# Performance work log

Measured on AMD Instinct MI355X. Metric: run time of the kernel, lower is better.

## Reference

```python
import jax, jax.numpy as jnp
import numpy as np

NP, NA, H, K, TAU = 4096, 2048, 128, 5, 1.0
NODE_N = {'paper': NP, 'author': NA}
RELS = [('pp', 'paper', 'paper'), ('aa', 'author', 'author'),
        ('pa', 'paper', 'author'), ('ap', 'author', 'paper')]


def setup_inputs():
    key = jax.random.key(0)
    ks = jax.random.split(key, 32)
    f32 = jnp.float32
    def nrm(k, shape, scale=1.0):
        return jax.random.normal(k, shape, f32) * scale
    Epp, Eaa, Epa, Eap = 131072, 65536, 131072, 131072
    inp = {
        'x_paper': nrm(ks[0], (NP, H)),
        'x_author': nrm(ks[1], (NA, H)),
        'ei_pp': jax.random.randint(ks[2], (2, Epp), 0, NP, dtype=jnp.int32),
        'ei_aa': jax.random.randint(ks[3], (2, Eaa), 0, NA, dtype=jnp.int32),
        'ei_pa': jnp.stack([jax.random.randint(ks[4], (Epa,), 0, NP, dtype=jnp.int32),
                            jax.random.randint(ks[5], (Epa,), 0, NA, dtype=jnp.int32)]),
        'ei_ap': jnp.stack([jax.random.randint(ks[6], (Eap,), 0, NA, dtype=jnp.int32),
                            jax.random.randint(ks[7], (Eap,), 0, NP, dtype=jnp.int32)]),
        'batch_paper': jnp.zeros((NP,), jnp.int32),
        'batch_author': jnp.zeros((NA,), jnp.int32),
        'index': 7,
    }
    s = H ** -0.5
    i = 8
    for t in ('paper', 'author'):
        for l in (0, 1):
            inp['Wself_%s%d' % (t, l)] = nrm(ks[i], (H, H), s); i += 1
    for r, _, _ in RELS:
        for l in (0, 1):
            inp['W%s%d' % (r, l)] = nrm(ks[i], (H, H), s); i += 1
    for r in ('pp', 'aa'):
        inp['Wep1_%s' % r] = nrm(ks[i], (2 * H, 256), (2 * H) ** -0.5); i += 1
        inp['bep1_%s' % r] = jnp.zeros((256,), f32)
        inp['Wep2_%s' % r] = nrm(ks[i], (256, 2), 256 ** -0.5); i += 1
        inp['bep2_%s' % r] = jnp.zeros((2,), f32)
    inp['Wc'] = nrm(ks[i], (H, 5), s)
    inp['bc'] = jnp.zeros((5,), f32)
    return inp


def _mean_agg(msg, dst, n):
    s = jax.ops.segment_sum(msg, dst, num_segments=n)
    c = jax.ops.segment_sum(jnp.ones((msg.shape[0], 1), msg.dtype), dst, num_segments=n)
    return s / jnp.maximum(c, 1.0)


def _gnn(x, ei, p, single, edge_attn=None):
    # 2-layer relation-typed mean-aggregation hetero GNN.
    h = dict(x)
    for l in (0, 1):
        nh = {}
        for t in ('paper', 'author'):
            agg = h[t] @ p['Wself_%s%d' % (t, l)]
            for r, s_t, d_t in RELS:
                if d_t != t or (single and s_t != d_t):
                    continue
                src, dst = ei[r][0], ei[r][1]
                msg = h[s_t][src] @ p['W%s%d' % (r, l)]  # [E, H]
                if edge_attn is not None and r in edge_attn:
                    msg = msg * edge_attn[r][:, None]
                agg = agg + _mean_agg(msg, dst, NODE_N[t])
            nh[t] = jax.nn.relu(agg)
        h = nh
    return h


def _edge_pred(h, ei, p, r, t):
    src, dst = ei[r][0], ei[r][1]
    e = jnp.concatenate([h[t][src], h[t][dst]], axis=-1)  # [E, 2H]
    e = jax.nn.relu(e @ p['Wep1_%s' % r] + p['bep1_%s' % r])
    return e @ p['Wep2_%s' % r] + p['bep2_%s' % r]  # [E, 2]


def _gumbel_topk(logits, mask, k, tau, key):
    # Masked straight-through top-k gumbel-softmax (row-wise, hard=True).
    u = jax.random.uniform(key, logits.shape, logits.dtype, 1e-10, 1.0)
    g = -jnp.log(-jnp.log(u))
    y = jnp.where(mask, (logits + g) / tau, -1e9)
    soft = jax.nn.softmax(y, axis=-1)
    _, idx = jax.lax.top_k(soft, k)  # [N, k]
    rows = jnp.arange(logits.shape[0])[:, None]
    hard = jnp.zeros_like(soft).at[rows, idx].set(1.0)
    return hard - jax.lax.stop_gradient(soft) + soft


def _prune(h, ei, p, r, t, n, key):
    pred = _edge_pred(h, ei, p, r, t)[:, 0]
    src, dst = ei[r][0], ei[r][1]
    # sparse_coo_tensor(...).to_dense(): duplicates coalesce by sum
    A = jnp.zeros((n, n), pred.dtype).at[src, dst].add(pred)
    S = _gumbel_topk(A, A > 0, K, TAU, key)
    return S[src, dst]


def _forward(p, ints):
    x = {'paper': p['x_paper'], 'author': p['x_author']}
    ei = {'pp': ints['ei_pp'], 'aa': ints['ei_aa'], 'pa': ints['ei_pa'], 'ap': ints['ei_ap']}
    h1 = _gnn(x, ei, p, single=True)
    kpp, kaa = jax.random.split(jax.random.key(42))
    w_pp = _prune(h1, ei, p, 'pp', 'paper', NP, kpp)
    w_aa = _prune(h1, ei, p, 'aa', 'author', NA, kaa)
    h2 = _gnn(x, ei, p, single=False, edge_attn={'pp': w_pp, 'aa': w_aa})
    pool = h2['paper'][ints['index']].reshape(1, -1)
    y_hat = pool @ p['Wc'] + p['bc']
    return y_hat, w_pp, w_aa


def reference(x_paper, x_author, ei_pp, ei_aa, ei_pa, ei_ap, batch_paper, batch_author, index,
              Wself_paper0, Wself_paper1, Wself_author0, Wself_author1,
              Wpp0, Wpp1, Waa0, Waa1, Wpa0, Wpa1, Wap0, Wap1,
              Wep1_pp, bep1_pp, Wep2_pp, bep2_pp, Wep1_aa, bep1_aa, Wep2_aa, bep2_aa,
              Wc, bc):
    p = dict(x_paper=x_paper, x_author=x_author,
             Wself_paper0=Wself_paper0, Wself_paper1=Wself_paper1,
             Wself_author0=Wself_author0, Wself_author1=Wself_author1,
             Wpp0=Wpp0, Wpp1=Wpp1, Waa0=Waa0, Waa1=Waa1,
             Wpa0=Wpa0, Wpa1=Wpa1, Wap0=Wap0, Wap1=Wap1,
             Wep1_pp=Wep1_pp, bep1_pp=bep1_pp, Wep2_pp=Wep2_pp, bep2_pp=bep2_pp,
             Wep1_aa=Wep1_aa, bep1_aa=bep1_aa, Wep2_aa=Wep2_aa, bep2_aa=bep2_aa,
             Wc=Wc, bc=bc)
    ints = dict(ei_pp=ei_pp, ei_aa=ei_aa, ei_pa=ei_pa, ei_ap=ei_ap, index=index)
    return _forward(p, ints)
```

## Files before the change

kernel.cpp:

```cpp
#include <hip/hip_runtime.h>
#include <stdint.h>


namespace {

constexpr int NPn = 4096;
constexpr int NAn = 2048;
constexpr int Hh  = 128;
constexpr int EPPc = 131072;
constexpr int EAAc = 65536;
constexpr int KSEL = 5;
constexpr int BSLOT = 128;


__host__ __device__ static inline void tf2x32(uint32_t k0, uint32_t k1,
                                              uint32_t& x0, uint32_t& x1) {
  uint32_t ks2 = k0 ^ k1 ^ 0x1BD11BDAu;
  x0 += k0; x1 += k1;
#define TF_R(r) { x0 += x1; x1 = (x1 << (r)) | (x1 >> (32 - (r))); x1 ^= x0; }
  TF_R(13) TF_R(15) TF_R(26) TF_R(6)
  x0 += k1;  x1 += ks2 + 1u;
  TF_R(17) TF_R(29) TF_R(16) TF_R(24)
  x0 += ks2; x1 += k0 + 2u;
  TF_R(13) TF_R(15) TF_R(26) TF_R(6)
  x0 += k0;  x1 += k1 + 3u;
  TF_R(17) TF_R(29) TF_R(16) TF_R(24)
  x0 += k1;  x1 += ks2 + 4u;
  TF_R(13) TF_R(15) TF_R(26) TF_R(6)
  x0 += ks2; x1 += k0 + 5u;
#undef TF_R
}

__global__ __launch_bounds__(256) void scatter_kernel(
    const int* src_pp, const int* dst_pp, const int* src_aa, const int* dst_aa,
    const int* src_pa, const int* dst_pa, const int* src_ap, const int* dst_ap,
    int* cnt, int* entries)
{
  int i = blockIdx.x * 256 + threadIdx.x;
  int key, pl;
  if (i < 131072) {
    int e = i;
    key = 0 + dst_pp[e]; pl = (src_pp[e] << 18) | e;
  } else if (i < 196608) {
    int e = i - 131072;
    key = 4096 + dst_aa[e]; pl = (src_aa[e] << 16) | e;
  } else if (i < 327680) {
    int e = i - 196608;
    key = 6144 + dst_pa[e]; pl = src_pa[e];
  } else if (i < 458752) {
    int e = i - 327680;
    key = 8192 + dst_ap[e]; pl = src_ap[e];
  } else if (i < 589824) {
    int e = i - 458752;
    key = 12288 + src_pp[e]; pl = (dst_pp[e] << 18) | e;
  } else if (i < 655360) {
    int e = i - 589824;
    key = 16384 + src_aa[e]; pl = (dst_aa[e] << 16) | e;
  } else return;
  int pos = atomicAdd(&cnt[key], 1);
  if (pos < BSLOT) entries[key * BSLOT + pos] = pl;
}

struct AggSeg { const float* h; const float* w; float* M; int cntOff; int shift; };
struct AggArgs { AggSeg s[4]; int start[5]; int nseg; };

__global__ __launch_bounds__(256) void multi_agg(AggArgs a, const int* __restrict__ cnt,
                                                 const int* __restrict__ entries)
{
  int g = blockIdx.x * 8 + (threadIdx.x >> 5);
  int fl = (threadIdx.x & 31) << 2;
  if (g >= a.start[a.nseg]) return;
  int si = 0;
  while (si < a.nseg - 1 && g >= a.start[si + 1]) ++si;
  AggSeg sg = a.s[si];
  int node = g - a.start[si];
  int deg = cnt[sg.cntOff + node];
  const int* ent = entries + (size_t)(sg.cntOff + node) * BSLOT;
  int b = 0, e = deg;
  const float* h = sg.h;
  int sh = sg.shift;
  float ax = 0.f, ay = 0.f, az = 0.f, aw = 0.f;
  if (sg.w) {
    unsigned mask = (1u << sh) - 1u;
    int k = b;
    for (; k + 3 < e; k += 4) {
      unsigned p0 = (unsigned)ent[k], p1 = (unsigned)ent[k + 1];
      unsigned p2 = (unsigned)ent[k + 2], p3 = (unsigned)ent[k + 3];
      float w0 = sg.w[p0 & mask], w1 = sg.w[p1 & mask];
      float w2v = sg.w[p2 & mask], w3 = sg.w[p3 & mask];
      float4 v0, v1, v2, v3;
      if (w0 != 0.f) v0 = *(const float4*)&h[(size_t)(p0 >> sh) * Hh + fl];
      if (w1 != 0.f) v1 = *(const float4*)&h[(size_t)(p1 >> sh) * Hh + fl];
      if (w2v != 0.f) v2 = *(const float4*)&h[(size_t)(p2 >> sh) * Hh + fl];
      if (w3 != 0.f) v3 = *(const float4*)&h[(size_t)(p3 >> sh) * Hh + fl];
      if (w0 != 0.f) { ax += v0.x; ay += v0.y; az += v0.z; aw += v0.w; }
      if (w1 != 0.f) { ax += v1.x; ay += v1.y; az += v1.z; aw += v1.w; }
      if (w2v != 0.f) { ax += v2.x; ay += v2.y; az += v2.z; aw += v2.w; }
      if (w3 != 0.f) { ax += v3.x; ay += v3.y; az += v3.z; aw += v3.w; }
    }
    for (; k < e; ++k) {
      unsigned pl = (unsigned)ent[k];
      float wt = sg.w[pl & mask];
      if (wt != 0.f) {
        float4 v = *(const float4*)&h[(size_t)(pl >> sh) * Hh + fl];
        ax += v.x; ay += v.y; az += v.z; aw += v.w;
      }
    }
  } else {
    int k = b;
    for (; k + 7 < e; k += 8) {
      unsigned p0 = (unsigned)ent[k],     p1 = (unsigned)ent[k + 1];
      unsigned p2 = (unsigned)ent[k + 2], p3 = (unsigned)ent[k + 3];
      unsigned p4 = (unsigned)ent[k + 4], p5 = (unsigned)ent[k + 5];
      unsigned p6 = (unsigned)ent[k + 6], p7 = (unsigned)ent[k + 7];
      float4 v0 = *(const float4*)&h[(size_t)(p0 >> sh) * Hh + fl];
      float4 v1 = *(const float4*)&h[(size_t)(p1 >> sh) * Hh + fl];
      float4 v2 = *(const float4*)&h[(size_t)(p2 >> sh) * Hh + fl];
      float4 v3 = *(const float4*)&h[(size_t)(p3 >> sh) * Hh + fl];
      float4 v4 = *(const float4*)&h[(size_t)(p4 >> sh) * Hh + fl];
      float4 v5 = *(const float4*)&h[(size_t)(p5 >> sh) * Hh + fl];
      float4 v6 = *(const float4*)&h[(size_t)(p6 >> sh) * Hh + fl];
      float4 v7 = *(const float4*)&h[(size_t)(p7 >> sh) * Hh + fl];
      ax += v0.x; ay += v0.y; az += v0.z; aw += v0.w;
      ax += v1.x; ay += v1.y; az += v1.z; aw += v1.w;
      ax += v2.x; ay += v2.y; az += v2.z; aw += v2.w;
      ax += v3.x; ay += v3.y; az += v3.z; aw += v3.w;
      ax += v4.x; ay += v4.y; az += v4.z; aw += v4.w;
      ax += v5.x; ay += v5.y; az += v5.z; aw += v5.w;
      ax += v6.x; ay += v6.y; az += v6.z; aw += v6.w;
      ax += v7.x; ay += v7.y; az += v7.z; aw += v7.w;
    }
    for (; k < e; ++k) {
      unsigned pl = (unsigned)ent[k];
      float4 v = *(const float4*)&h[(size_t)(pl >> sh) * Hh + fl];
      ax += v.x; ay += v.y; az += v.z; aw += v.w;
    }
  }
  float cd = fmaxf((float)deg, 1.0f);
  float4 o; o.x = ax / cd; o.y = ay / cd; o.z = az / cd; o.w = aw / cd;
  *(float4*)&sg.M[(size_t)node * Hh + fl] = o;
}

struct GDesc {
  const float* A0; const float* W0; const float* A1; const float* W1;
  const float* A2; const float* W2; float* C; int M; int N; int parts; int relu;
};
struct GArgs { GDesc d[4]; int bstart[5]; int nd; };

__global__ __launch_bounds__(256) void gemm_b(GArgs g)
{
  __shared__ __align__(16) float As[2][32][68];
  __shared__ __align__(16) float Ws[2][32][68];
  int blk = blockIdx.x;
  int di = 0;
  while (di < g.nd - 1 && blk >= g.bstart[di + 1]) ++di;
  GDesc D = g.d[di];
  int local = blk - g.bstart[di];
  int nTiles = D.N >> 6;
  int bx = local % nTiles;
  int by = local / nTiles;
  int m0 = by << 6, n0 = bx << 6;
  int N = D.N;
  int tid = threadIdx.x;
  int tr = tid >> 4, tc = tid & 15;
  int r = tid >> 3, f = tid & 7;
  float acc[4][4] = {{0.f}};
  const float* Ap[3] = {D.A0, D.A1, D.A2};
  const float* Wp[3] = {D.W0, D.W1, D.W2};
  int T = D.parts << 2;

  float4 va0, va1, vw0, vw1;
  auto ldchunk = [&](int t) {
    const float* A = Ap[t >> 2]; const float* W = Wp[t >> 2];
    int k0 = (t & 3) << 5;
    va0 = *(const float4*)&A[(size_t)(m0 + r) * 128 + k0 + f * 4];
    va1 = *(const float4*)&A[(size_t)(m0 + r + 32) * 128 + k0 + f * 4];
    vw0 = *(const float4*)&W[(size_t)(k0 + r) * N + n0 + f * 4];
    vw1 = *(const float4*)&W[(size_t)(k0 + r) * N + n0 + f * 4 + 32];
  };
  auto stchunk = [&](int buf) {
    As[buf][f * 4 + 0][r] = va0.x; As[buf][f * 4 + 1][r] = va0.y;
    As[buf][f * 4 + 2][r] = va0.z; As[buf][f * 4 + 3][r] = va0.w;
    As[buf][f * 4 + 0][r + 32] = va1.x; As[buf][f * 4 + 1][r + 32] = va1.y;
    As[buf][f * 4 + 2][r + 32] = va1.z; As[buf][f * 4 + 3][r + 32] = va1.w;
    *(float4*)&Ws[buf][r][f * 4] = vw0;
    *(float4*)&Ws[buf][r][f * 4 + 32] = vw1;
  };

  ldchunk(0);
  stchunk(0);
  __syncthreads();
  for (int t = 0; t < T; ++t) {
    int cur = t & 1;
    bool more = (t + 1 < T);
    if (more) ldchunk(t + 1);
#pragma unroll
    for (int k = 0; k < 32; ++k) {
      float4 a = *(const float4*)&As[cur][k][tr * 4];
      float4 b = *(const float4*)&Ws[cur][k][tc * 4];
      acc[0][0] += a.x * b.x; acc[0][1] += a.x * b.y; acc[0][2] += a.x * b.z; acc[0][3] += a.x * b.w;
      acc[1][0] += a.y * b.x; acc[1][1] += a.y * b.y; acc[1][2] += a.y * b.z; acc[1][3] += a.y * b.w;
      acc[2][0] += a.z * b.x; acc[2][1] += a.z * b.y; acc[2][2] += a.z * b.z; acc[2][3] += a.z * b.w;
      acc[3][0] += a.w * b.x; acc[3][1] += a.w * b.y; acc[3][2] += a.w * b.z; acc[3][3] += a.w * b.w;
    }
    if (more) stchunk(cur ^ 1);
    __syncthreads();
  }
#pragma unroll
  for (int i = 0; i < 4; ++i) {
    float4 v;
    v.x = acc[i][0]; v.y = acc[i][1]; v.z = acc[i][2]; v.w = acc[i][3];
    if (D.relu) {
      v.x = fmaxf(v.x, 0.f); v.y = fmaxf(v.y, 0.f);
      v.z = fmaxf(v.z, 0.f); v.w = fmaxf(v.w, 0.f);
    }
    *(float4*)&D.C[(size_t)(m0 + tr * 4 + i) * N + n0 + tc * 4] = v;
  }
}

__global__ __launch_bounds__(256) void row_topk(
    const float* __restrict__ P1pp, const float* __restrict__ P2pp,
    const float* __restrict__ b1pp, const float* __restrict__ W2pp,
    const float* __restrict__ b2pp,
    const float* __restrict__ P1aa, const float* __restrict__ P2aa,
    const float* __restrict__ b1aa, const float* __restrict__ W2aa,
    const float* __restrict__ b2aa,
    const int* __restrict__ cnt, const int* __restrict__ entries,
    float* __restrict__ w_pp, float* __restrict__ w_aa,
    uint32_t kpp0, uint32_t kpp1, uint32_t kaa0, uint32_t kaa1)
{
  __shared__ float P1s[256], b1s[256], w2s[256];
  __shared__ int   dS[128];
  __shared__ float pS[128];
  __shared__ int   sel5[KSEL];
  int blk = blockIdx.x, tid = threadIdx.x;
  int lane = tid & 63, wv = tid >> 6;
  int row, Ncols, shift, co; unsigned mask;
  const float* P1; const float* P2; const float* b1; const float* W2; const float* b2;
  float* wout; uint32_t k0, k1;
  if (blk < NPn) {
    row = blk; Ncols = NPn; shift = 18; mask = 0x3FFFFu; co = 12288;
    P1 = P1pp; P2 = P2pp; b1 = b1pp; W2 = W2pp; b2 = b2pp;
    wout = w_pp; k0 = kpp0; k1 = kpp1;
  } else {
    row = blk - NPn; Ncols = NAn; shift = 16; mask = 0xFFFFu; co = 16384;
    P1 = P1aa; P2 = P2aa; b1 = b1aa; W2 = W2aa; b2 = b2aa;
    wout = w_aa; k0 = kaa0; k1 = kaa1;
  }
  const int* ent = entries + (size_t)(co + row) * BSLOT;
  int deg = cnt[co + row];
  P1s[tid] = P1[(size_t)row * 256 + tid];
  b1s[tid] = b1[tid];
  w2s[tid] = W2[tid * 2];
  __syncthreads();
  float bias2 = b2[0];
  int j = lane << 2;
  for (int k = wv * 4; k < deg; k += 16) {
    int n = deg - k; if (n > 4) n = 4;
    unsigned pl0 = (unsigned)ent[k];
    unsigned pl1 = (n > 1) ? (unsigned)ent[k + 1] : pl0;
    unsigned pl2 = (n > 2) ? (unsigned)ent[k + 2] : pl0;
    unsigned pl3 = (n > 3) ? (unsigned)ent[k + 3] : pl0;
    int d0 = (int)(pl0 >> shift), d1 = (int)(pl1 >> shift);
    int d2 = (int)(pl2 >> shift), d3 = (int)(pl3 >> shift);
    float4 q0 = *(const float4*)&P2[(size_t)d0 * 256 + j];
    float4 q1 = *(const float4*)&P2[(size_t)d1 * 256 + j];
    float4 q2 = *(const float4*)&P2[(size_t)d2 * 256 + j];
    float4 q3 = *(const float4*)&P2[(size_t)d3 * 256 + j];
    float pa = P1s[j + 0], pb = P1s[j + 1], pc = P1s[j + 2], pd = P1s[j + 3];
    float ba = b1s[j + 0], bb = b1s[j + 1], bc_ = b1s[j + 2], bd = b1s[j + 3];
    float wa = w2s[j + 0], wb = w2s[j + 1], wc = w2s[j + 2], wd = w2s[j + 3];
    float s0 = fmaxf(pa + q0.x + ba, 0.f) * wa + fmaxf(pb + q0.y + bb, 0.f) * wb +
               fmaxf(pc + q0.z + bc_, 0.f) * wc + fmaxf(pd + q0.w + bd, 0.f) * wd;
    float s1 = fmaxf(pa + q1.x + ba, 0.f) * wa + fmaxf(pb + q1.y + bb, 0.f) * wb +
               fmaxf(pc + q1.z + bc_, 0.f) * wc + fmaxf(pd + q1.w + bd, 0.f) * wd;
    float s2 = fmaxf(pa + q2.x + ba, 0.f) * wa + fmaxf(pb + q2.y + bb, 0.f) * wb +
               fmaxf(pc + q2.z + bc_, 0.f) * wc + fmaxf(pd + q2.w + bd, 0.f) * wd;
    float s3 = fmaxf(pa + q3.x + ba, 0.f) * wa + fmaxf(pb + q3.y + bb, 0.f) * wb +
               fmaxf(pc + q3.z + bc_, 0.f) * wc + fmaxf(pd + q3.w + bd, 0.f) * wd;
    for (int off = 32; off; off >>= 1) {
      s0 += __shfl_down(s0, off);
      s1 += __shfl_down(s1, off);
      s2 += __shfl_down(s2, off);
      s3 += __shfl_down(s3, off);
    }
    if (lane == 0) {
      dS[k] = d0; pS[k] = s0 + bias2;
      if (n > 1) { dS[k + 1] = d1; pS[k + 1] = s1 + bias2; }
      if (n > 2) { dS[k + 2] = d2; pS[k + 2] = s2 + bias2; }
      if (n > 3) { dS[k + 3] = d3; pS[k + 3] = s3 + bias2; }
    }
  }
  __syncthreads();
  if (deg > 0 && wv == 0) {
    int   e0 = (lane < deg) ? dS[lane] : -1;
    float q0v = (lane < deg) ? pS[lane] : 0.f;
    bool  two = (deg > 64);
    int   e1 = -1; float q1v = 0.f;
    if (two && 64 + lane < deg) { e1 = dS[64 + lane]; q1v = pS[64 + lane]; }
    float a0 = 0.f, a1 = 0.f;
    bool lead0 = (e0 >= 0), lead1 = (e1 >= 0);
    for (int j2 = 0; j2 < deg; ++j2) {
      int bj; float bp;
      if (j2 < 64) { bj = __shfl(e0, j2); bp = __shfl(q0v, j2); }
      else         { bj = __shfl(e1, j2 - 64); bp = __shfl(q1v, j2 - 64); }
      if (e0 >= 0 && bj == e0) { a0 += bp; if (j2 < lane) lead0 = false; }
      if (e1 >= 0 && bj == e1) { a1 += bp; if (j2 < 64 + lane) lead1 = false; }
    }
    uint32_t rowbase = (uint32_t)row * (uint32_t)Ncols;
    float y0 = -1e9f, y1 = -1e9f;
    bool c0 = lead0 && (a0 > 0.f);
    if (c0) {
      uint32_t x0 = 0u, x1 = rowbase + (uint32_t)e0;
      tf2x32(k0, k1, x0, x1);
      uint32_t bits = x0 ^ x1;
      float fv = __uint_as_float((bits >> 9) | 0x3f800000u) - 1.0f;
      float u = fmaxf(1e-10f, fv + 1e-10f);
      y0 = a0 + (-logf(-logf(u)));
    }
    bool c1 = lead1 && (a1 > 0.f);
    if (c1) {
      uint32_t x0 = 0u, x1 = rowbase + (uint32_t)e1;
      tf2x32(k0, k1, x0, x1);
      uint32_t bits = x0 ^ x1;
      float fv = __uint_as_float((bits >> 9) | 0x3f800000u) - 1.0f;
      float u = fmaxf(1e-10f, fv + 1e-10f);
      y1 = a1 + (-logf(-logf(u)));
    }
    int cnt2 = __popcll(__ballot(c0)) + __popcll(__ballot(c1));
    int nsel = cnt2 < KSEL ? cnt2 : KSEL;
    for (int it = 0; it < nsel; ++it) {
      float best; int bc;
      if (y1 > y0 || (y1 == y0 && (unsigned)e1 < (unsigned)e0)) { best = y1; bc = e1; }
      else { best = y0; bc = e0; }
      for (int m = 32; m; m >>= 1) {
        float ov = __shfl_xor(best, m); int oc = __shfl_xor(bc, m);
        if (ov > best || (ov == best && (unsigned)oc < (unsigned)bc)) { best = ov; bc = oc; }
      }
      if (lane == 0) sel5[it] = bc;
      if (e0 == bc) y0 = -3.0e38f;
      if (e1 == bc) y1 = -3.0e38f;
    }
    if (nsel < KSEL && lane == 0) {
      int c = 0;
      for (int it = nsel; it < KSEL; ++it) {
        for (;;) {
          bool used = false;
          for (int q = 0; q < it; ++q) used |= (sel5[q] == c);
          if (!used) break;
          ++c;
        }
        sel5[it] = c++;
      }
    }
  }
  __syncthreads();
  for (int k = tid; k < deg; k += 256) {
    unsigned pl = (unsigned)ent[k];
    int d = (int)(pl >> shift);
    int e = (int)(pl & mask);
    float v = 0.f;
#pragma unroll
    for (int q = 0; q < KSEL; ++q) v = (sel5[q] == d) ? 1.f : v;
    wout[e] = v;
  }
}

__global__ __launch_bounds__(128) void final_kernel(
    const float* __restrict__ hp, const float* __restrict__ ha,
    const int* __restrict__ idxPtr, const float* __restrict__ wpp,
    const int* __restrict__ cnt, const int* __restrict__ entries,
    const float* __restrict__ Wself, const float* __restrict__ Wpp,
    const float* __restrict__ Wap,
    const float* __restrict__ Wc, const float* __restrict__ bc,
    float* __restrict__ out)
{
  __shared__ float selfr[128], mpp[128], mapr[128], t[128];
  int tid = threadIdx.x;
  int idx = idxPtr[0];
  selfr[tid] = hp[(size_t)idx * 128 + tid];
  {
    int deg = cnt[idx];
    const int* ent = entries + (size_t)idx * BSLOT;
    float acc = 0.f;
    for (int k = 0; k < deg; ++k) {
      unsigned pl = (unsigned)ent[k];
      int s = (int)(pl >> 18);
      int e = (int)(pl & 0x3FFFFu);
      acc += wpp[e] * hp[(size_t)s * 128 + tid];
    }
    mpp[tid] = acc / fmaxf((float)deg, 1.0f);
  }
  {
    int deg = cnt[8192 + idx];
    const int* ent = entries + (size_t)(8192 + idx) * BSLOT;
    float acc = 0.f;
    for (int k = 0; k < deg; ++k) {
      int s = ent[k];
      acc += ha[(size_t)s * 128 + tid];
    }
    mapr[tid] = acc / fmaxf((float)deg, 1.0f);
  }
  __syncthreads();
  float s = 0.f;
  for (int m = 0; m < 128; ++m) {
    s += selfr[m] * Wself[m * 128 + tid] + mpp[m] * Wpp[m * 128 + tid] +
         mapr[m] * Wap[m * 128 + tid];
  }
  t[tid] = fmaxf(s, 0.f);
  __syncthreads();
  if (tid < 5) {
    float y = bc[tid];
    for (int k = 0; k < 128; ++k) y += t[k] * Wc[k * 5 + tid];
    out[tid] = y;
  }
}

}

extern "C" void kernel_launch(void* const* d_in, const int* in_sizes, int n_in,
                              void* d_out, int out_size, void* d_ws, size_t ws_size,
                              hipStream_t stream)
{
  (void)in_sizes; (void)n_in; (void)out_size; (void)ws_size;
  const float* x_p = (const float*)d_in[0];
  const float* x_a = (const float*)d_in[1];
  const int* ei_pp = (const int*)d_in[2];
  const int* ei_aa = (const int*)d_in[3];
  const int* ei_pa = (const int*)d_in[4];
  const int* ei_ap = (const int*)d_in[5];
  const int* idxPtr = (const int*)d_in[8];
  const float* Wself_p0 = (const float*)d_in[9];
  const float* Wself_p1 = (const float*)d_in[10];
  const float* Wself_a0 = (const float*)d_in[11];
  const float* Wself_a1 = (const float*)d_in[12];
  const float* Wpp0 = (const float*)d_in[13]; const float* Wpp1 = (const float*)d_in[14];
  const float* Waa0 = (const float*)d_in[15]; const float* Waa1 = (const float*)d_in[16];
  const float* Wpa0 = (const float*)d_in[17];
  const float* Wap0 = (const float*)d_in[19]; const float* Wap1 = (const float*)d_in[20];
  const float* Wep1_pp = (const float*)d_in[21]; const float* bep1_pp = (const float*)d_in[22];
  const float* Wep2_pp = (const float*)d_in[23]; const float* bep2_pp = (const float*)d_in[24];
  const float* Wep1_aa = (const float*)d_in[25]; const float* bep1_aa = (const float*)d_in[26];
  const float* Wep2_aa = (const float*)d_in[27]; const float* bep2_aa = (const float*)d_in[28];
  const float* Wc = (const float*)d_in[29]; const float* bc = (const float*)d_in[30];

  float* out = (float*)d_out;
  float* w_pp_out = out + 5;
  float* w_aa_out = out + 5 + EPPc;

  const int* src_pp = ei_pp;  const int* dst_pp = ei_pp + EPPc;
  const int* src_aa = ei_aa;  const int* dst_aa = ei_aa + EAAc;
  const int* src_pa = ei_pa;  const int* dst_pa = ei_pa + 131072;
  const int* src_ap = ei_ap;  const int* dst_ap = ei_ap + 131072;

  char* p = (char*)d_ws;
  auto alloc = [&](size_t bytes) -> void* {
    void* r = (void*)p;
    p += (bytes + 255) & ~(size_t)255;
    return r;
  };
  int* cnt     = (int*)alloc(18432 * sizeof(int));
  int* entries = (int*)alloc((size_t)18432 * BSLOT * sizeof(int));
  float* Mpp  = (float*)alloc((size_t)NPn * Hh * sizeof(float));
  float* Maa  = (float*)alloc((size_t)NAn * Hh * sizeof(float));
  float* Mpa  = (float*)alloc((size_t)NAn * Hh * sizeof(float));
  float* Map  = (float*)alloc((size_t)NPn * Hh * sizeof(float));
  float* h1p0 = (float*)alloc((size_t)NPn * Hh * sizeof(float));
  float* h1a0 = (float*)alloc((size_t)NAn * Hh * sizeof(float));
  float* h1p1 = (float*)alloc((size_t)NPn * Hh * sizeof(float));
  float* h1a1 = (float*)alloc((size_t)NAn * Hh * sizeof(float));
  float* h2p0 = (float*)alloc((size_t)NPn * Hh * sizeof(float));
  float* h2a0 = (float*)alloc((size_t)NAn * Hh * sizeof(float));
  float* P1pp = (float*)alloc((size_t)NPn * 256 * sizeof(float));
  float* P2pp = (float*)alloc((size_t)NPn * 256 * sizeof(float));
  float* P1aa = (float*)alloc((size_t)NAn * 256 * sizeof(float));
  float* P2aa = (float*)alloc((size_t)NAn * 256 * sizeof(float));

  const int CO_PPD = 0, CO_AAD = 4096, CO_PAD = 6144, CO_APD = 8192;

  hipMemsetAsync(cnt, 0, 18432 * sizeof(int), stream);
  scatter_kernel<<<2560, 256, 0, stream>>>(src_pp, dst_pp, src_aa, dst_aa,
                                           src_pa, dst_pa, src_ap, dst_ap,
                                           cnt, entries);

  {
    AggArgs a{};
    a.s[0] = {x_p, nullptr, Mpp, CO_PPD, 18};
    a.s[1] = {x_a, nullptr, Maa, CO_AAD, 16};
    a.s[2] = {x_a, nullptr, Map, CO_APD, 0};
    a.s[3] = {x_p, nullptr, Mpa, CO_PAD, 0};
    a.start[0] = 0; a.start[1] = NPn; a.start[2] = NPn + NAn;
    a.start[3] = 2 * NPn + NAn; a.start[4] = 2 * NPn + 2 * NAn; a.nseg = 4;
    multi_agg<<<(2 * NPn + 2 * NAn) / 8, 256, 0, stream>>>(a, cnt, entries);
  }
  {
    GArgs g{};
    g.d[0] = {x_p, Wself_p0, Mpp, Wpp0, nullptr, nullptr, h1p0, NPn, 128, 2, 1};
    g.d[1] = {x_a, Wself_a0, Maa, Waa0, nullptr, nullptr, h1a0, NAn, 128, 2, 1};
    g.bstart[0] = 0; g.bstart[1] = 128; g.bstart[2] = 192; g.nd = 2;
    gemm_b<<<192, 256, 0, stream>>>(g);
  }
  {
    AggArgs a{};
    a.s[0] = {h1p0, nullptr, Mpp, CO_PPD, 18};
    a.s[1] = {h1a0, nullptr, Maa, CO_AAD, 16};
    a.start[0] = 0; a.start[1] = NPn; a.start[2] = NPn + NAn; a.nseg = 2;
    multi_agg<<<(NPn + NAn) / 8, 256, 0, stream>>>(a, cnt, entries);
  }
  {
    GArgs g{};
    g.d[0] = {h1p0, Wself_p1, Mpp, Wpp1, nullptr, nullptr, h1p1, NPn, 128, 2, 1};
    g.d[1] = {h1a0, Wself_a1, Maa, Waa1, nullptr, nullptr, h1a1, NAn, 128, 2, 1};
    g.bstart[0] = 0; g.bstart[1] = 128; g.bstart[2] = 192; g.nd = 2;
    gemm_b<<<192, 256, 0, stream>>>(g);
  }

  {
    GArgs g{};
    g.d[0] = {h1p1, Wep1_pp,             nullptr, nullptr, nullptr, nullptr, P1pp, NPn, 256, 1, 0};
    g.d[1] = {h1p1, Wep1_pp + 128 * 256, nullptr, nullptr, nullptr, nullptr, P2pp, NPn, 256, 1, 0};
    g.d[2] = {h1a1, Wep1_aa,             nullptr, nullptr, nullptr, nullptr, P1aa, NAn, 256, 1, 0};
    g.d[3] = {h1a1, Wep1_aa + 128 * 256, nullptr, nullptr, nullptr, nullptr, P2aa, NAn, 256, 1, 0};
    g.bstart[0] = 0; g.bstart[1] = 256; g.bstart[2] = 512; g.bstart[3] = 640;
    g.bstart[4] = 768; g.nd = 4;
    gemm_b<<<768, 256, 0, stream>>>(g);
  }

  uint32_t kpp0, kpp1, kaa0, kaa1;
  { uint32_t a0 = 0, a1 = 0; tf2x32(0u, 42u, a0, a1); kpp0 = a0; kpp1 = a1; }
  { uint32_t a0 = 0, a1 = 1; tf2x32(0u, 42u, a0, a1); kaa0 = a0; kaa1 = a1; }

  row_topk<<<NPn + NAn, 256, 0, stream>>>(P1pp, P2pp, bep1_pp, Wep2_pp, bep2_pp,
                                          P1aa, P2aa, bep1_aa, Wep2_aa, bep2_aa,
                                          cnt, entries, w_pp_out, w_aa_out,
                                          kpp0, kpp1, kaa0, kaa1);

  {
    AggArgs a{};
    a.s[0] = {x_p, w_pp_out, Mpp, CO_PPD, 18};
    a.s[1] = {x_a, w_aa_out, Maa, CO_AAD, 16};
    a.start[0] = 0; a.start[1] = NPn; a.start[2] = NPn + NAn; a.nseg = 2;
    multi_agg<<<(NPn + NAn) / 8, 256, 0, stream>>>(a, cnt, entries);
  }
  {
    GArgs g{};
    g.d[0] = {x_p, Wself_p0, Mpp, Wpp0, Map, Wap0, h2p0, NPn, 128, 3, 1};
    g.d[1] = {x_a, Wself_a0, Maa, Waa0, Mpa, Wpa0, h2a0, NAn, 128, 3, 1};
    g.bstart[0] = 0; g.bstart[1] = 128; g.bstart[2] = 192; g.nd = 2;
    gemm_b<<<192, 256, 0, stream>>>(g);
  }

  final_kernel<<<1, 128, 0, stream>>>(h2p0, h2a0, idxPtr, w_pp_out,
                                      cnt, entries,
                                      Wself_p1, Wpp1, Wap1, Wc, bc, out);
}
```

Measured before the change: 360.6 us.

## Fuse mean aggregation with per-node GEMMs and edge-predictor projection

Replaces the separate multi_agg and tiled gemm_b launches with one fused_layer kernel. Each 8-node block gathers neighbour means into shared memory, then multiplies self features and aggregates by the 128x128 weights, and in layer 1 also computes the Wep1 projections directly. This removes launches and the global round trips of the intermediate M and h1 buffers. In exchange the GEMM runs with tiny 8-row tiles that reload the full weight matrices per block, and the Wep1 projection reads its weights straight from global memory with no reuse, which may cost more than the dense tiled GEMM did.

```diff
diff --git a/kernel.cpp b/kernel.cpp
--- a/kernel.cpp
+++ b/kernel.cpp
@@ -61,161 +61,163 @@
   if (pos < BSLOT) entries[key * BSLOT + pos] = pl;
 }
 
-struct AggSeg { const float* h; const float* w; float* M; int cntOff; int shift; };
-struct AggArgs { AggSeg s[4]; int start[5]; int nseg; };
-
-__global__ __launch_bounds__(256) void multi_agg(AggArgs a, const int* __restrict__ cnt,
-                                                 const int* __restrict__ entries)
+struct FDesc {
+  const float* gsrc; const float* wArr; int cntOff; int shift;
+  float* Mout;
+  const float* Aself; const float* W0; const float* W1;
+  const float* A2;  const float* W2;
+  float* C; int relu;
+  const float* WP; float* P1; float* P2;
+};
+struct FArgs { FDesc d[4]; int bstart[5]; int nd; };
+
+__global__ __launch_bounds__(256) void fused_layer(FArgs fa, const int* __restrict__ cnt,
+                                                   const int* __restrict__ entries)
 {
-  int g = blockIdx.x * 8 + (threadIdx.x >> 5);
-  int fl = (threadIdx.x & 31) << 2;
-  if (g >= a.start[a.nseg]) return;
-  int si = 0;
-  while (si < a.nseg - 1 && g >= a.start[si + 1]) ++si;
-  AggSeg sg = a.s[si];
-  int node = g - a.start[si];
-  int deg = cnt[sg.cntOff + node];
-  const int* ent = entries + (size_t)(sg.cntOff + node) * BSLOT;
-  int b = 0, e = deg;
-  const float* h = sg.h;
-  int sh = sg.shift;
-  float ax = 0.f, ay = 0.f, az = 0.f, aw = 0.f;
-  if (sg.w) {
-    unsigned mask = (1u << sh) - 1u;
-    int k = b;
-    for (; k + 3 < e; k += 4) {
-      unsigned p0 = (unsigned)ent[k], p1 = (unsigned)ent[k + 1];
-      unsigned p2 = (unsigned)ent[k + 2], p3 = (unsigned)ent[k + 3];
-      float w0 = sg.w[p0 & mask], w1 = sg.w[p1 & mask];
-      float w2v = sg.w[p2 & mask], w3 = sg.w[p3 & mask];
-      float4 v0, v1, v2, v3;
-      if (w0 != 0.f) v0 = *(const float4*)&h[(size_t)(p0 >> sh) * Hh + fl];
-      if (w1 != 0.f) v1 = *(const float4*)&h[(size_t)(p1 >> sh) * Hh + fl];
-      if (w2v != 0.f) v2 = *(const float4*)&h[(size_t)(p2 >> sh) * Hh + fl];
-      if (w3 != 0.f) v3 = *(const float4*)&h[(size_t)(p3 >> sh) * Hh + fl];
-      if (w0 != 0.f) { ax += v0.x; ay += v0.y; az += v0.z; aw += v0.w; }
-      if (w1 != 0.f) { ax += v1.x; ay += v1.y; az += v1.z; aw += v1.w; }
-      if (w2v != 0.f) { ax += v2.x; ay += v2.y; az += v2.z; aw += v2.w; }
-      if (w3 != 0.f) { ax += v3.x; ay += v3.y; az += v3.z; aw += v3.w; }
-    }
-    for (; k < e; ++k) {
-      unsigned pl = (unsigned)ent[k];
-      float wt = sg.w[pl & mask];
-      if (wt != 0.f) {
+  __shared__ __align__(16) float Ms[8][128];
+  __shared__ __align__(16) float Xs[8][128];
+  __shared__ __align__(16) float Zs[8][128];
+  __shared__ __align__(16) float Ws[32][128];
+  int blk = blockIdx.x, tid = threadIdx.x;
+  int di = 0;
+  while (di < fa.nd - 1 && blk >= fa.bstart[di + 1]) ++di;
+  FDesc D = fa.d[di];
+  int node0 = (blk - fa.bstart[di]) * 8;
+  {
+    int hw = tid >> 5;
+    int node = node0 + hw;
+    int fl = (tid & 31) << 2;
+    int deg = cnt[D.cntOff + node];
+    const int* ent = entries + (size_t)(D.cntOff + node) * BSLOT;
+    const float* h = D.gsrc;
+    int sh = D.shift;
+    float ax = 0.f, ay = 0.f, az = 0.f, aw = 0.f;
+    if (D.wArr) {
+      unsigned mask = (1u << sh) - 1u;
+      int k = 0;
+      for (; k + 3 < deg; k += 4) {
+        unsigned p0 = (unsigned)ent[k], p1 = (unsigned)ent[k + 1];
+        unsigned p2 = (unsigned)ent[k + 2], p3 = (unsigned)ent[k + 3];
+        float w0 = D.wArr[p0 & mask], w1 = D.wArr[p1 & mask];
+        float w2v = D.wArr[p2 & mask], w3 = D.wArr[p3 & mask];
+        float4 v0, v1, v2, v3;
+        if (w0 != 0.f) v0 = *(const float4*)&h[(size_t)(p0 >> sh) * Hh + fl];
+        if (w1 != 0.f) v1 = *(const float4*)&h[(size_t)(p1 >> sh) * Hh + fl];
+        if (w2v != 0.f) v2 = *(const float4*)&h[(size_t)(p2 >> sh) * Hh + fl];
+        if (w3 != 0.f) v3 = *(const float4*)&h[(size_t)(p3 >> sh) * Hh + fl];
+        if (w0 != 0.f) { ax += v0.x; ay += v0.y; az += v0.z; aw += v0.w; }
+        if (w1 != 0.f) { ax += v1.x; ay += v1.y; az += v1.z; aw += v1.w; }
+        if (w2v != 0.f) { ax += v2.x; ay += v2.y; az += v2.z; aw += v2.w; }
+        if (w3 != 0.f) { ax += v3.x; ay += v3.y; az += v3.z; aw += v3.w; }
+      }
+      for (; k < deg; ++k) {
+        unsigned pl = (unsigned)ent[k];
+        float wt = D.wArr[pl & mask];
+        if (wt != 0.f) {
+          float4 v = *(const float4*)&h[(size_t)(pl >> sh) * Hh + fl];
+          ax += v.x; ay += v.y; az += v.z; aw += v.w;
+        }
+      }
+    } else {
+      int k = 0;
+      for (; k + 7 < deg; k += 8) {
+        unsigned p0 = (unsigned)ent[k],     p1 = (unsigned)ent[k + 1];
+        unsigned p2 = (unsigned)ent[k + 2], p3 = (unsigned)ent[k + 3];
+        unsigned p4 = (unsigned)ent[k + 4], p5 = (unsigned)ent[k + 5];
+        unsigned p6 = (unsigned)ent[k + 6], p7 = (unsigned)ent[k + 7];
+        float4 v0 = *(const float4*)&h[(size_t)(p0 >> sh) * Hh + fl];
+        float4 v1 = *(const float4*)&h[(size_t)(p1 >> sh) * Hh + fl];
+        float4 v2 = *(const float4*)&h[(size_t)(p2 >> sh) * Hh + fl];
+        float4 v3 = *(const float4*)&h[(size_t)(p3 >> sh) * Hh + fl];
+        float4 v4 = *(const float4*)&h[(size_t)(p4 >> sh) * Hh + fl];
+        float4 v5 = *(const float4*)&h[(size_t)(p5 >> sh) * Hh + fl];
+        float4 v6 = *(const float4*)&h[(size_t)(p6 >> sh) * Hh + fl];
+        float4 v7 = *(const float4*)&h[(size_t)(p7 >> sh) * Hh + fl];
+        ax += v0.x; ay += v0.y; az += v0.z; aw += v0.w;
+        ax += v1.x; ay += v1.y; az += v1.z; aw += v1.w;
+        ax += v2.x; ay += v2.y; az += v2.z; aw += v2.w;
+        ax += v3.x; ay += v3.y; az += v3.z; aw += v3.w;
+        ax += v4.x; ay += v4.y; az += v4.z; aw += v4.w;
+        ax += v5.x; ay += v5.y; az += v5.z; aw += v5.w;
+        ax += v6.x; ay += v6.y; az += v6.z; aw += v6.w;
+        ax += v7.x; ay += v7.y; az += v7.z; aw += v7.w;
+      }
+      for (; k < deg; ++k) {
+        unsigned pl = (unsigned)ent[k];
         float4 v = *(const float4*)&h[(size_t)(pl >> sh) * Hh + fl];
         ax += v.x; ay += v.y; az += v.z; aw += v.w;
       }
     }
-  } else {
-    int k = b;
-    for (; k + 7 < e; k += 8) {
-      unsigned p0 = (unsigned)ent[k],     p1 = (unsigned)ent[k + 1];
-      unsigned p2 = (unsigned)ent[k + 2], p3 = (unsigned)ent[k + 3];
-      unsigned p4 = (unsigned)ent[k + 4], p5 = (unsigned)ent[k + 5];
-      unsigned p6 = (unsigned)ent[k + 6], p7 = (unsigned)ent[k + 7];
-      float4 v0 = *(const float4*)&h[(size_t)(p0 >> sh) * Hh + fl];
-      float4 v1 = *(const float4*)&h[(size_t)(p1 >> sh) * Hh + fl];
-      float4 v2 = *(const float4*)&h[(size_t)(p2 >> sh) * Hh + fl];
-      float4 v3 = *(const float4*)&h[(size_t)(p3 >> sh) * Hh + fl];
-      float4 v4 = *(const float4*)&h[(size_t)(p4 >> sh) * Hh + fl];
-      float4 v5 = *(const float4*)&h[(size_t)(p5 >> sh) * Hh + fl];
-      float4 v6 = *(const float4*)&h[(size_t)(p6 >> sh) * Hh + fl];
-      float4 v7 = *(const float4*)&h[(size_t)(p7 >> sh) * Hh + fl];
-      ax += v0.x; ay += v0.y; az += v0.z; aw += v0.w;
-      ax += v1.x; ay += v1.y; az += v1.z; aw += v1.w;
-      ax += v2.x; ay += v2.y; az += v2.z; aw += v2.w;
-      ax += v3.x; ay += v3.y; az += v3.z; aw += v3.w;
-      ax += v4.x; ay += v4.y; az += v4.z; aw += v4.w;
-      ax += v5.x; ay += v5.y; az += v5.z; aw += v5.w;
-      ax += v6.x; ay += v6.y; az += v6.z; aw += v6.w;
-      ax += v7.x; ay += v7.y; az += v7.z; aw += v7.w;
-    }
-    for (; k < e; ++k) {
-      unsigned pl = (unsigned)ent[k];
-      float4 v = *(const float4*)&h[(size_t)(pl >> sh) * Hh + fl];
-      ax += v.x; ay += v.y; az += v.z; aw += v.w;
-    }
-  }
-  float cd = fmaxf((float)deg, 1.0f);
-  float4 o; o.x = ax / cd; o.y = ay / cd; o.z = az / cd; o.w = aw / cd;
-  *(float4*)&sg.M[(size_t)node * Hh + fl] = o;
-}
-
-struct GDesc {
-  const float* A0; const float* W0; const float* A1; const float* W1;
-  const float* A2; const float* W2; float* C; int M; int N; int parts; int relu;
-};
-struct GArgs { GDesc d[4]; int bstart[5]; int nd; };
-
-__global__ __launch_bounds__(256) void gemm_b(GArgs g)
-{
-  __shared__ __align__(16) float As[2][32][68];
-  __shared__ __align__(16) float Ws[2][32][68];
-  int blk = blockIdx.x;
-  int di = 0;
-  while (di < g.nd - 1 && blk >= g.bstart[di + 1]) ++di;
-  GDesc D = g.d[di];
-  int local = blk - g.bstart[di];
-  int nTiles = D.N >> 6;
-  int bx = local % nTiles;
-  int by = local / nTiles;
-  int m0 = by << 6, n0 = bx << 6;
-  int N = D.N;
-  int tid = threadIdx.x;
-  int tr = tid >> 4, tc = tid & 15;
-  int r = tid >> 3, f = tid & 7;
-  float acc[4][4] = {{0.f}};
-  const float* Ap[3] = {D.A0, D.A1, D.A2};
-  const float* Wp[3] = {D.W0, D.W1, D.W2};
-  int T = D.parts << 2;
-
-  float4 va0, va1, vw0, vw1;
-  auto ldchunk = [&](int t) {
-    const float* A = Ap[t >> 2]; const float* W = Wp[t >> 2];
-    int k0 = (t & 3) << 5;
-    va0 = *(const float4*)&A[(size_t)(m0 + r) * 128 + k0 + f * 4];
-    va1 = *(const float4*)&A[(size_t)(m0 + r + 32) * 128 + k0 + f * 4];
-    vw0 = *(const float4*)&W[(size_t)(k0 + r) * N + n0 + f * 4];
-    vw1 = *(const float4*)&W[(size_t)(k0 + r) * N + n0 + f * 4 + 32];
-  };
-  auto stchunk = [&](int buf) {
-    As[buf][f * 4 + 0][r] = va0.x; As[buf][f * 4 + 1][r] = va0.y;
-    As[buf][f * 4 + 2][r] = va0.z; As[buf][f * 4 + 3][r] = va0.w;
-    As[buf][f * 4 + 0][r + 32] = va1.x; As[buf][f * 4 + 1][r + 32] = va1.y;
-    As[buf][f * 4 + 2][r + 32] = va1.z; As[buf][f * 4 + 3][r + 32] = va1.w;
-    *(float4*)&Ws[buf][r][f * 4] = vw0;
-    *(float4*)&Ws[buf][r][f * 4 + 32] = vw1;
-  };
-
-  ldchunk(0);
-  stchunk(0);
-  __syncthreads();
-  for (int t = 0; t < T; ++t) {
-    int cur = t & 1;
-    bool more = (t + 1 < T);
-    if (more) ldchunk(t + 1);
-#pragma unroll
-    for (int k = 0; k < 32; ++k) {
-      float4 a = *(const float4*)&As[cur][k][tr * 4];
-      float4 b = *(const float4*)&Ws[cur][k][tc * 4];
-      acc[0][0] += a.x * b.x; acc[0][1] += a.x * b.y; acc[0][2] += a.x * b.z; acc[0][3] += a.x * b.w;
-      acc[1][0] += a.y * b.x; acc[1][1] += a.y * b.y; acc[1][2] += a.y * b.z; acc[1][3] += a.y * b.w;
-      acc[2][0] += a.z * b.x; acc[2][1] += a.z * b.y; acc[2][2] += a.z * b.z; acc[2][3] += a.z * b.w;
-      acc[3][0] += a.w * b.x; acc[3][1] += a.w * b.y; acc[3][2] += a.w * b.z; acc[3][3] += a.w * b.w;
-    }
-    if (more) stchunk(cur ^ 1);
-    __syncthreads();
-  }
-#pragma unroll
-  for (int i = 0; i < 4; ++i) {
-    float4 v;
-    v.x = acc[i][0]; v.y = acc[i][1]; v.z = acc[i][2]; v.w = acc[i][3];
-    if (D.relu) {
-      v.x = fmaxf(v.x, 0.f); v.y = fmaxf(v.y, 0.f);
-      v.z = fmaxf(v.z, 0.f); v.w = fmaxf(v.w, 0.f);
-    }
-    *(float4*)&D.C[(size_t)(m0 + tr * 4 + i) * N + n0 + tc * 4] = v;
-  }
+    float cd = fmaxf((float)deg, 1.0f);
+    float4 o; o.x = ax / cd; o.y = ay / cd; o.z = az / cd; o.w = aw / cd;
+    if (D.W0 == nullptr) {
+      *(float4*)&D.Mout[(size_t)node * Hh + fl] = o;
+    } else {
+      *(float4*)&Ms[hw][fl] = o;
+    }
+  }
+  if (D.W0 == nullptr) return;
+  {
+    int rm = tid >> 5, cq = (tid & 31) << 2;
+    *(float4*)&Xs[rm][cq] = *(const float4*)&D.Aself[(size_t)(node0 + rm) * 128 + cq];
+    if (D.A2)
+      *(float4*)&Zs[rm][cq] = *(const float4*)&D.A2[(size_t)(node0 + rm) * 128 + cq];
+  }
+  int m = tid >> 5, nq = tid & 31;
+  float4 accv = {0.f, 0.f, 0.f, 0.f};
+  int parts = D.A2 ? 3 : 2;
+  for (int p = 0; p < parts; ++p) {
+    const float* W = (p == 0) ? D.W0 : (p == 1) ? D.W1 : D.W2;
+    for (int c = 0; c < 4; ++c) {
+      __syncthreads();
+      {
+        int r = tid >> 3, f = (tid & 7) << 4;
+        const float* srcp = &W[(size_t)(c * 32 + r) * 128 + f];
+        *(float4*)&Ws[r][f]      = *(const float4*)&srcp[0];
+        *(float4*)&Ws[r][f + 4]  = *(const float4*)&srcp[4];
+        *(float4*)&Ws[r][f + 8]  = *(const float4*)&srcp[8];
+        *(float4*)&Ws[r][f + 12] = *(const float4*)&srcp[12];
+      }
+      __syncthreads();
+#define KCHUNK(AR)                                              \
+      _Pragma("unroll")                                         \
+      for (int k = 0; k < 32; ++k) {                            \
+        float a = AR[m][c * 32 + k];                            \
+        float4 wv = *(const float4*)&Ws[k][nq << 2];            \
+        accv.x += a * wv.x; accv.y += a * wv.y;                 \
+        accv.z += a * wv.z; accv.w += a * wv.w;                 \
+      }
+      if (p == 0) { KCHUNK(Xs) } else if (p == 1) { KCHUNK(Ms) } else { KCHUNK(Zs) }
+#undef KCHUNK
+    }
+  }
+  if (D.relu) {
+    accv.x = fmaxf(accv.x, 0.f); accv.y = fmaxf(accv.y, 0.f);
+    accv.z = fmaxf(accv.z, 0.f); accv.w = fmaxf(accv.w, 0.f);
+  }
+  if (D.C)
+    *(float4*)&D.C[(size_t)(node0 + m) * 128 + (nq << 2)] = accv;
+  if (D.WP == nullptr) return;
+  __syncthreads();
+  *(float4*)&Xs[m][nq << 2] = accv;
+  __syncthreads();
+  int c0 = nq << 3;
+  float4 p1a = {0,0,0,0}, p1b = {0,0,0,0}, p2a = {0,0,0,0}, p2b = {0,0,0,0};
+  for (int k = 0; k < 128; ++k) {
+    float a = Xs[m][k];
+    const float* w1 = &D.WP[(size_t)k * 256 + c0];
+    const float* w2 = &D.WP[(size_t)(128 + k) * 256 + c0];
+    float4 u1a = *(const float4*)&w1[0], u1b = *(const float4*)&w1[4];
+    float4 u2a = *(const float4*)&w2[0], u2b = *(const float4*)&w2[4];
+    p1a.x += a * u1a.x; p1a.y += a * u1a.y; p1a.z += a * u1a.z; p1a.w += a * u1a.w;
+    p1b.x += a * u1b.x; p1b.y += a * u1b.y; p1b.z += a * u1b.z; p1b.w += a * u1b.w;
+    p2a.x += a * u2a.x; p2a.y += a * u2a.y; p2a.z += a * u2a.z; p2a.w += a * u2a.w;
+    p2b.x += a * u2b.x; p2b.y += a * u2b.y; p2b.z += a * u2b.z; p2b.w += a * u2b.w;
+  }
+  *(float4*)&D.P1[(size_t)(node0 + m) * 256 + c0]     = p1a;
+  *(float4*)&D.P1[(size_t)(node0 + m) * 256 + c0 + 4] = p1b;
+  *(float4*)&D.P2[(size_t)(node0 + m) * 256 + c0]     = p2a;
+  *(float4*)&D.P2[(size_t)(node0 + m) * 256 + c0 + 4] = p2b;
 }
 
 __global__ __launch_bounds__(256) void row_topk(
@@ -333,8 +335,8 @@
       float best; int bc;
       if (y1 > y0 || (y1 == y0 && (unsigned)e1 < (unsigned)e0)) { best = y1; bc = e1; }
       else { best = y0; bc = e0; }
-      for (int m = 32; m; m >>= 1) {
-        float ov = __shfl_xor(best, m); int oc = __shfl_xor(bc, m);
+      for (int mm = 32; mm; mm >>= 1) {
+        float ov = __shfl_xor(best, mm); int oc = __shfl_xor(bc, mm);
         if (ov > best || (ov == best && (unsigned)oc < (unsigned)bc)) { best = ov; bc = oc; }
       }
       if (lane == 0) sel5[it] = bc;
@@ -461,14 +463,10 @@
   };
   int* cnt     = (int*)alloc(18432 * sizeof(int));
   int* entries = (int*)alloc((size_t)18432 * BSLOT * sizeof(int));
-  float* Mpp  = (float*)alloc((size_t)NPn * Hh * sizeof(float));
-  float* Maa  = (float*)alloc((size_t)NAn * Hh * sizeof(float));
+  float* Map  = (float*)alloc((size_t)NPn * Hh * sizeof(float));
   float* Mpa  = (float*)alloc((size_t)NAn * Hh * sizeof(float));
-  float* Map  = (float*)alloc((size_t)NPn * Hh * sizeof(float));
   float* h1p0 = (float*)alloc((size_t)NPn * Hh * sizeof(float));
   float* h1a0 = (float*)alloc((size_t)NAn * Hh * sizeof(float));
-  float* h1p1 = (float*)alloc((size_t)NPn * Hh * sizeof(float));
-  float* h1a1 = (float*)alloc((size_t)NAn * Hh * sizeof(float));
   float* h2p0 = (float*)alloc((size_t)NPn * Hh * sizeof(float));
   float* h2a0 = (float*)alloc((size_t)NAn * Hh * sizeof(float));
   float* P1pp = (float*)alloc((size_t)NPn * 256 * sizeof(float));
@@ -484,46 +482,34 @@
                                            cnt, entries);
 
   {
-    AggArgs a{};
-    a.s[0] = {x_p, nullptr, Mpp, CO_PPD, 18};
-    a.s[1] = {x_a, nullptr, Maa, CO_AAD, 16};
-    a.s[2] = {x_a, nullptr, Map, CO_APD, 0};
-    a.s[3] = {x_p, nullptr, Mpa, CO_PAD, 0};
-    a.start[0] = 0; a.start[1] = NPn; a.start[2] = NPn + NAn;
-    a.start[3] = 2 * NPn + NAn; a.start[4] = 2 * NPn + 2 * NAn; a.nseg = 4;
-    multi_agg<<<(2 * NPn + 2 * NAn) / 8, 256, 0, stream>>>(a, cnt, entries);
-  }
-  {
-    GArgs g{};
-    g.d[0] = {x_p, Wself_p0, Mpp, Wpp0, nullptr, nullptr, h1p0, NPn, 128, 2, 1};
-    g.d[1] = {x_a, Wself_a0, Maa, Waa0, nullptr, nullptr, h1a0, NAn, 128, 2, 1};
-    g.bstart[0] = 0; g.bstart[1] = 128; g.bstart[2] = 192; g.nd = 2;
-    gemm_b<<<192, 256, 0, stream>>>(g);
-  }
-  {
-    AggArgs a{};
-    a.s[0] = {h1p0, nullptr, Mpp, CO_PPD, 18};
-    a.s[1] = {h1a0, nullptr, Maa, CO_AAD, 16};
-    a.start[0] = 0; a.start[1] = NPn; a.start[2] = NPn + NAn; a.nseg = 2;
-    multi_agg<<<(NPn + NAn) / 8, 256, 0, stream>>>(a, cnt, entries);
-  }
-  {
-    GArgs g{};
-    g.d[0] = {h1p0, Wself_p1, Mpp, Wpp1, nullptr, nullptr, h1p1, NPn, 128, 2, 1};
-    g.d[1] = {h1a0, Wself_a1, Maa, Waa1, nullptr, nullptr, h1a1, NAn, 128, 2, 1};
-    g.bstart[0] = 0; g.bstart[1] = 128; g.bstart[2] = 192; g.nd = 2;
-    gemm_b<<<192, 256, 0, stream>>>(g);
-  }
-
-  {
-    GArgs g{};
-    g.d[0] = {h1p1, Wep1_pp,             nullptr, nullptr, nullptr, nullptr, P1pp, NPn, 256, 1, 0};
-    g.d[1] = {h1p1, Wep1_pp + 128 * 256, nullptr, nullptr, nullptr, nullptr, P2pp, NPn, 256, 1, 0};
-    g.d[2] = {h1a1, Wep1_aa,             nullptr, nullptr, nullptr, nullptr, P1aa, NAn, 256, 1, 0};
-    g.d[3] = {h1a1, Wep1_aa + 128 * 256, nullptr, nullptr, nullptr, nullptr, P2aa, NAn, 256, 1, 0};
-    g.bstart[0] = 0; g.bstart[1] = 256; g.bstart[2] = 512; g.bstart[3] = 640;
-    g.bstart[4] = 768; g.nd = 4;
-    gemm_b<<<768, 256, 0, stream>>>(g);
+    FArgs fa{};
+    fa.d[0] = {x_p, nullptr, CO_PPD, 18, nullptr,
+               x_p, Wself_p0, Wpp0, nullptr, nullptr, h1p0, 1,
+               nullptr, nullptr, nullptr};
+    fa.d[1] = {x_a, nullptr, CO_AAD, 16, nullptr,
+               x_a, Wself_a0, Waa0, nullptr, nullptr, h1a0, 1,
+               nullptr, nullptr, nullptr};
+    fa.d[2] = {x_a, nullptr, CO_APD, 0, Map,
+               nullptr, nullptr, nullptr, nullptr, nullptr, nullptr, 0,
+               nullptr, nullptr, nullptr};
+    fa.d[3] = {x_p, nullptr, CO_PAD, 0, Mpa,
+               nullptr, nullptr, nullptr, nullptr, nullptr, nullptr, 0,
+               nullptr, nullptr, nullptr};
+    fa.bstart[0] = 0; fa.bstart[1] = 512; fa.bstart[2] = 768;
+    fa.bstart[3] = 1280; fa.bstart[4] = 1536; fa.nd = 4;
+    fused_layer<<<1536, 256, 0, stream>>>(fa, cnt, entries);
+  }
+
+  {
+    FArgs fa{};
+    fa.d[0] = {h1p0, nullptr, CO_PPD, 18, nullptr,
+               h1p0, Wself_p1, Wpp1, nullptr, nullptr, nullptr, 1,
+               Wep1_pp, P1pp, P2pp};
+    fa.d[1] = {h1a0, nullptr, CO_AAD, 16, nullptr,
+               h1a0, Wself_a1, Waa1, nullptr, nullptr, nullptr, 1,
+               Wep1_aa, P1aa, P2aa};
+    fa.bstart[0] = 0; fa.bstart[1] = 512; fa.bstart[2] = 768; fa.nd = 2;
+    fused_layer<<<768, 256, 0, stream>>>(fa, cnt, entries);
   }
 
   uint32_t kpp0, kpp1, kaa0, kaa1;
@@ -536,18 +522,15 @@
                                           kpp0, kpp1, kaa0, kaa1);
 
   {
-    AggArgs a{};
-    a.s[0] = {x_p, w_pp_out, Mpp, CO_PPD, 18};
-    a.s[1] = {x_a, w_aa_out, Maa, CO_AAD, 16};
-    a.start[0] = 0; a.start[1] = NPn; a.start[2] = NPn + NAn; a.nseg = 2;
-    multi_agg<<<(NPn + NAn) / 8, 256, 0, stream>>>(a, cnt, entries);
-  }
-  {
-    GArgs g{};
-    g.d[0] = {x_p, Wself_p0, Mpp, Wpp0, Map, Wap0, h2p0, NPn, 128, 3, 1};
-    g.d[1] = {x_a, Wself_a0, Maa, Waa0, Mpa, Wpa0, h2a0, NAn, 128, 3, 1};
-    g.bstart[0] = 0; g.bstart[1] = 128; g.bstart[2] = 192; g.nd = 2;
-    gemm_b<<<192, 256, 0, stream>>>(g);
+    FArgs fa{};
+    fa.d[0] = {x_p, w_pp_out, CO_PPD, 18, nullptr,
+               x_p, Wself_p0, Wpp0, Map, Wap0, h2p0, 1,
+               nullptr, nullptr, nullptr};
+    fa.d[1] = {x_a, w_aa_out, CO_AAD, 16, nullptr,
+               x_a, Wself_a0, Waa0, Mpa, Wpa0, h2a0, 1,
+               nullptr, nullptr, nullptr};
+    fa.bstart[0] = 0; fa.bstart[1] = 512; fa.bstart[2] = 768; fa.nd = 2;
+    fused_layer<<<768, 256, 0, stream>>>(fa, cnt, entries);
   }
 
   final_kernel<<<1, 128, 0, stream>>>(h2p0, h2a0, idxPtr, w_pp_out,
```

Result: no change. 359.7 us (-0.3%).
